# Kernel tuning notes

Hardware: AMD Instinct MI355X
Metric: run time of the kernel (lower is better)

The kernel has to match this reference:

```python
import jax, jax.numpy as jnp
import numpy as np

NUM_EMBEDDINGS = 8192
EMBEDDING_DIM = 512
BETA = 0.25


def setup_inputs() -> dict:
    key = jax.random.key(0)
    k1, k2 = jax.random.split(key)
    x = jax.random.normal(k1, (16, 1024, EMBEDDING_DIM), dtype=jnp.float32)
    # torch.nn.init.uniform_ -> U[0, 1)
    embeddings = jax.random.uniform(k2, (NUM_EMBEDDINGS, EMBEDDING_DIM), dtype=jnp.float32)
    return {"x": x, "embeddings": embeddings}


def reference(x, embeddings):
    input_shape = x.shape
    flat = x.reshape(-1, EMBEDDING_DIM)                      # [N, D]
    sim = jnp.matmul(flat, embeddings.T)                     # [N, K]
    s1 = jnp.sum(flat * flat, axis=1, keepdims=True)         # [N, 1]
    s2 = jnp.sum(embeddings * embeddings, axis=1)            # [K]
    distances = s1 + s2 - 2.0 * sim                          # [N, K]
    idx = jnp.argmin(distances, axis=1)                      # [N]
    # direct gather (math-equivalent to one-hot @ codebook)
    quantized = embeddings[idx].reshape(input_shape)
    sg = jax.lax.stop_gradient
    commitment_loss = BETA * jnp.mean((sg(quantized) - x) ** 2)
    codebook_loss = jnp.mean((quantized - sg(x)) ** 2)
    loss = commitment_loss + codebook_loss
    out = x + sg(quantized - x)                              # straight-through
    return (out, quantized, loss)
```

## Files before the change

### kernel.cpp

```cpp
#include <hip/hip_runtime.h>

#define DIM 512
#define N_ROWS 16384
#define K_CODES 8192
#define BK 32
#define TM 128
#define TN 128
#define NG (K_CODES / TN)
#define OUT_ELEMS (N_ROWS * DIM)
#define MARGIN 0.125f
#define RESCAN_CHUNK 1024
#define RESCAN_NCHUNK (K_CODES / RESCAN_CHUNK)
#define RESCAN_ROWS 8
#define NT (DIM / BK)

typedef _Float16 f16;
typedef _Float16 f16x8 __attribute__((ext_vector_type(8)));
typedef float f32x4 __attribute__((ext_vector_type(4)));

__device__ __forceinline__ unsigned long long pack_di(float d, int i) {
  unsigned u = __float_as_uint(d);
  u = (u & 0x80000000u) ? ~u : (u | 0x80000000u);
  return ((unsigned long long)u << 32) | (unsigned)i;
}

__global__ __launch_bounds__(256) void vq_split_kernel(const float* __restrict__ src,
                                                       f16* __restrict__ x16) {
  int i = (blockIdx.x * 256 + threadIdx.x) * 8;
  float4 v0 = *(const float4*)(src + i);
  float4 v1 = *(const float4*)(src + i + 4);
  float f[8] = {v0.x, v0.y, v0.z, v0.w, v1.x, v1.y, v1.z, v1.w};
  f16x8 h;
  #pragma unroll
  for (int j = 0; j < 8; ++j) h[j] = (f16)f[j];
  *(f16x8*)(x16 + i) = h;
}

__global__ __launch_bounds__(256) void vq_split_enorm_kernel(
    const float* __restrict__ emb, f16* __restrict__ e16,
    float* __restrict__ enorm, int* __restrict__ counter) {
  int gid  = blockIdx.x * 256 + threadIdx.x;
  if (gid == 0) *counter = 0;
  int code = gid >> 6;
  int lane = gid & 63;
  size_t off = (size_t)code * DIM + lane * 8;
  float4 v0 = *(const float4*)(emb + off);
  float4 v1 = *(const float4*)(emb + off + 4);
  float f[8] = {v0.x, v0.y, v0.z, v0.w, v1.x, v1.y, v1.z, v1.w};
  f16x8 h;
  float s = 0.0f;
  #pragma unroll
  for (int j = 0; j < 8; ++j) {
    h[j] = (f16)f[j];
    s = fmaf(f[j], f[j], s);
  }
  *(f16x8*)(e16 + off) = h;
  #pragma unroll
  for (int o = 32; o > 0; o >>= 1) s += __shfl_down(s, o);
  if (lane == 0) enorm[code] = s;
}

__device__ __forceinline__ void gl2lds16(const f16* g, f16* l) {
  __builtin_amdgcn_global_load_lds((const __attribute__((address_space(1))) unsigned int*)g,
                                   (__attribute__((address_space(3))) unsigned int*)l,
                                   16, 0, 0);
}

__device__ __forceinline__ void top2_merge(float& d1, int& i1, float& d2,
                                           float od1, int oi1, float od2) {
  if (od1 < d1 || (od1 == d1 && oi1 < i1)) {
    d2 = fminf(d1, od2);
    d1 = od1; i1 = oi1;
  } else {
    d2 = fminf(d2, od1);
  }
}

__global__ __launch_bounds__(256, 4) void vq_argmin_mfma_kernel(
    const f16* __restrict__ x16, const f16* __restrict__ e16,
    const float* __restrict__ enorm,
    float* __restrict__ cand_d1, int* __restrict__ cand_i1, float* __restrict__ cand_d2) {
  __shared__ __align__(16) f16 Ax[2][TM * BK];
  __shared__ __align__(16) f16 Be[2][TN * BK];
  __shared__ float red_d1[2][TM];
  __shared__ int   red_i1[2][TM];
  __shared__ float red_d2[2][TM];

  const int tid  = threadIdx.x;
  const int wave = tid >> 6;
  const int lane = tid & 63;
  const int bm = blockIdx.x, bn = blockIdx.y;
  const int wr = (wave >> 1) * 64;
  const int wc = (wave & 1) * 64;

  const f16* gsrc0;
  int ldoff;
  {
    const int srow = lane >> 2;
    const int scg  = ((lane & 3) ^ ((lane >> 3) & 3)) * 8;
    const int rowoff = (wave & 1) * 64;
    if (wave < 2) { gsrc0 = x16 + (size_t)(bm * TM + rowoff + srow) * DIM + scg; }
    else          { gsrc0 = e16 + (size_t)(bn * TN + rowoff + srow) * DIM + scg; }
    ldoff = rowoff * BK;
  }
  f16* dstA0 = (wave < 2) ? &Ax[0][ldoff] : &Be[0][ldoff];
  f16* dstA1 = (wave < 2) ? &Ax[1][ldoff] : &Be[1][ldoff];

  f32x4 acc[4][4];
  #pragma unroll
  for (int i = 0; i < 4; ++i)
    #pragma unroll
    for (int j = 0; j < 4; ++j)
      acc[i][j] = (f32x4){0.f, 0.f, 0.f, 0.f};

  const int fr = lane & 15;
  const int fq = lane >> 4;
  const int sw8 = (fq ^ ((fr >> 1) & 3)) * 8;

  #pragma unroll
  for (int i = 0; i < 4; ++i)
    gl2lds16(gsrc0 + (size_t)(16 * i) * DIM, dstA0 + (16 * i) * BK);
  __syncthreads();

  #pragma unroll 2
  for (int s = 0; s < NT; ++s) {
    const int cur = s & 1;
    if (s + 1 < NT) {
      f16* nb = cur ? dstA0 : dstA1;
      const int k1 = (s + 1) * BK;
      #pragma unroll
      for (int i = 0; i < 4; ++i)
        gl2lds16(gsrc0 + (size_t)(16 * i) * DIM + k1, nb + (16 * i) * BK);
    }

    const f16* A = cur ? &Ax[1][0] : &Ax[0][0];
    const f16* B = cur ? &Be[1][0] : &Be[0][0];
    f16x8 a[4], b[4];
    #pragma unroll
    for (int f = 0; f < 4; ++f) {
      a[f] = *(const f16x8*)&A[(wr + f * 16 + fr) * BK + sw8];
      b[f] = *(const f16x8*)&B[(wc + f * 16 + fr) * BK + sw8];
    }
    #pragma unroll
    for (int mf = 0; mf < 4; ++mf)
      #pragma unroll
      for (int nf = 0; nf < 4; ++nf)
        acc[mf][nf] = __builtin_amdgcn_mfma_f32_16x16x32_f16(a[mf], b[nf], acc[mf][nf], 0, 0, 0);

    __syncthreads();
  }

  float en[4];
  #pragma unroll
  for (int nf = 0; nf < 4; ++nf)
    en[nf] = enorm[bn * TN + wc + nf * 16 + fr];

  #pragma unroll
  for (int mf = 0; mf < 4; ++mf) {
    #pragma unroll
    for (int reg = 0; reg < 4; ++reg) {
      float d1 = 3.4e38f, d2 = 3.4e38f;
      int i1 = 0;
      #pragma unroll
      for (int nf = 0; nf < 4; ++nf) {
        float d = en[nf] - 2.0f * acc[mf][nf][reg];
        int ci = bn * TN + wc + nf * 16 + fr;
        if (d < d1) { d2 = d1; d1 = d; i1 = ci; }
        else if (d < d2) { d2 = d; }
      }
      #pragma unroll
      for (int m = 1; m <= 8; m <<= 1) {
        float od1 = __shfl_xor(d1, m, 16);
        int   oi1 = __shfl_xor(i1, m, 16);
        float od2 = __shfl_xor(d2, m, 16);
        top2_merge(d1, i1, d2, od1, oi1, od2);
      }
      if (fr == 0) {
        int row = wr + mf * 16 + fq * 4 + reg;
        red_d1[wave & 1][row] = d1;
        red_i1[wave & 1][row] = i1;
        red_d2[wave & 1][row] = d2;
      }
    }
  }
  __syncthreads();
  if (tid < TM) {
    float d1 = red_d1[0][tid]; int i1 = red_i1[0][tid]; float d2 = red_d2[0][tid];
    top2_merge(d1, i1, d2, red_d1[1][tid], red_i1[1][tid], red_d2[1][tid]);
    size_t o = (size_t)bn * N_ROWS + (size_t)bm * TM + tid;
    cand_d1[o] = d1; cand_i1[o] = i1; cand_d2[o] = d2;
  }
}

__global__ __launch_bounds__(256) void vq_merge2_kernel(
    const float* __restrict__ cd1, const int* __restrict__ ci1, const float* __restrict__ cd2,
    int* __restrict__ idx, int* __restrict__ flag,
    int* __restrict__ counter, int* __restrict__ flagged,
    unsigned long long* __restrict__ packed,
    float* __restrict__ loss_slot) {
  int r = blockIdx.x * 256 + threadIdx.x;
  if (r == 0) *loss_slot = 0.0f;
  float d1 = 3.4e38f, d2 = 3.4e38f;
  int i1 = 0;
  for (int g = 0; g < NG; ++g) {
    size_t o = (size_t)g * N_ROWS + r;
    top2_merge(d1, i1, d2, cd1[o], ci1[o], cd2[o]);
  }
  idx[r] = i1;
  int f = (d2 - d1 < MARGIN) ? 1 : 0;
  flag[r] = f;
  if (f) {
    packed[r] = 0xFFFFFFFFFFFFFFFFULL;
    int slot = atomicAdd(counter, 1);
    flagged[slot] = r;
  }
}

__global__ __launch_bounds__(256) void vq_rescan_kernel(
    const float* __restrict__ x, const float* __restrict__ emb,
    const float* __restrict__ enorm,
    const int* __restrict__ counter, const int* __restrict__ flagged,
    unsigned long long* __restrict__ packed) {
  __shared__ float4 xs[RESCAN_ROWS][DIM / 4];
  __shared__ unsigned long long wmin[4][RESCAN_ROWS];
  const int t  = threadIdx.x;
  const int wv = t >> 6, ln = t & 63;
  const int nflag   = counter[0];
  const int ngroups = (nflag + RESCAN_ROWS - 1) / RESCAN_ROWS;
  const int nitems  = ngroups * RESCAN_NCHUNK;
  for (int item = blockIdx.x; item < nitems; item += gridDim.x) {
    const int g  = item / RESCAN_NCHUNK;
    const int c0 = (item % RESCAN_NCHUNK) * RESCAN_CHUNK;
    __syncthreads();
    #pragma unroll
    for (int u = 0; u < 4; ++u) {
      int i4 = u * 256 + t;
      int j = i4 >> 7, k = i4 & 127;
      int rj = g * RESCAN_ROWS + j;
      if (rj < nflag) xs[j][k] = ((const float4*)(x + (size_t)flagged[rj] * DIM))[k];
    }
    __syncthreads();
    unsigned long long best[RESCAN_ROWS];
    #pragma unroll
    for (int j = 0; j < RESCAN_ROWS; ++j) best[j] = ~0ULL;
    #pragma unroll
    for (int cc = 0; cc < RESCAN_CHUNK / 256; ++cc) {
      const int c = c0 + cc * 256 + t;
      const float4* e4 = (const float4*)(emb + (size_t)c * DIM);
      float s0[RESCAN_ROWS], s1[RESCAN_ROWS], s2[RESCAN_ROWS], s3[RESCAN_ROWS];
      #pragma unroll
      for (int j = 0; j < RESCAN_ROWS; ++j) { s0[j] = s1[j] = s2[j] = s3[j] = 0.f; }
      for (int k = 0; k < DIM / 4; ++k) {
        float4 ev = e4[k];
        #pragma unroll
        for (int j = 0; j < RESCAN_ROWS; ++j) {
          float4 xv = xs[j][k];
          s0[j] = fmaf(xv.x, ev.x, s0[j]);
          s1[j] = fmaf(xv.y, ev.y, s1[j]);
          s2[j] = fmaf(xv.z, ev.z, s2[j]);
          s3[j] = fmaf(xv.w, ev.w, s3[j]);
        }
      }
      const float en = enorm[c];
      #pragma unroll
      for (int j = 0; j < RESCAN_ROWS; ++j) {
        float d = en - 2.0f * ((s0[j] + s1[j]) + (s2[j] + s3[j]));
        unsigned long long p = pack_di(d, c);
        if (p < best[j]) best[j] = p;
      }
    }
    #pragma unroll
    for (int j = 0; j < RESCAN_ROWS; ++j) {
      #pragma unroll
      for (int off = 32; off > 0; off >>= 1) {
        unsigned long long o = __shfl_down(best[j], off);
        if (o < best[j]) best[j] = o;
      }
    }
    if (ln == 0) {
      #pragma unroll
      for (int j = 0; j < RESCAN_ROWS; ++j) wmin[wv][j] = best[j];
    }
    __syncthreads();
    if (t < RESCAN_ROWS) {
      int rj = g * RESCAN_ROWS + t;
      if (rj < nflag) {
        unsigned long long m = wmin[0][t];
        if (wmin[1][t] < m) m = wmin[1][t];
        if (wmin[2][t] < m) m = wmin[2][t];
        if (wmin[3][t] < m) m = wmin[3][t];
        atomicMin(&packed[flagged[rj]], m);
      }
    }
  }
}

__global__ __launch_bounds__(256) void vq_gather_kernel(
    const float* __restrict__ x, const float* __restrict__ emb,
    const int* __restrict__ idx, const int* __restrict__ flag,
    const unsigned long long* __restrict__ packed,
    float* __restrict__ out, float* __restrict__ quant,
    float* __restrict__ loss_slot) {
  __shared__ float wsum[4];
  const int wave = threadIdx.x >> 6;
  const int lane = threadIdx.x & 63;
  const int row  = blockIdx.x * 4 + wave;
  const int code = flag[row] ? (int)(packed[row] & 0xFFFFFFFFu) : idx[row];
  const float4* xp = (const float4*)(x   + (size_t)row  * DIM + lane * 8);
  const float4* ep = (const float4*)(emb + (size_t)code * DIM + lane * 8);
  float s = 0.0f;
  #pragma unroll
  for (int t = 0; t < 2; ++t) {
    float4 xv = xp[t];
    float4 ev = ep[t];
    float dx = ev.x - xv.x, dy = ev.y - xv.y, dz = ev.z - xv.z, dw = ev.w - xv.w;
    s += dx * dx + dy * dy + dz * dz + dw * dw;
    ((float4*)(out   + (size_t)row * DIM + lane * 8))[t] = ev;
    ((float4*)(quant + (size_t)row * DIM + lane * 8))[t] = ev;
  }
  #pragma unroll
  for (int off = 32; off > 0; off >>= 1) s += __shfl_down(s, off);
  if (lane == 0) wsum[wave] = s;
  __syncthreads();
  if (threadIdx.x == 0) {
    float tot = wsum[0] + wsum[1] + wsum[2] + wsum[3];
    atomicAdd(loss_slot, tot * (1.25f / (float)OUT_ELEMS));
  }
}

extern "C" void kernel_launch(void* const* d_in, const int* in_sizes, int n_in,
                              void* d_out, int out_size, void* d_ws, size_t ws_size,
                              hipStream_t stream) {
  const float* x   = (const float*)d_in[0];
  const float* emb = (const float*)d_in[1];
  float* out   = (float*)d_out;
  float* quant = out + OUT_ELEMS;
  float* loss  = out + 2 * OUT_ELEMS;

  char* ws = (char*)d_ws;
  f16*   x16    = (f16*)(ws);
  f16*   e16    = (f16*)(ws + 16777216);
  float* enorm  = (float*)(ws + 25165824);
  float* cd1    = (float*)(ws + 25198592);
  int*   ci1    = (int*)  (ws + 29392896);
  float* cd2    = (float*)(ws + 33587200);
  int*   idx    = (int*)  (ws + 37781504);
  int*   flag   = (int*)  (ws + 37847040);
  int*   counter= (int*)  (ws + 37912576);
  int*   flagged= (int*)  (ws + 37912832);
  unsigned long long* packed = (unsigned long long*)(ws + 37978368);

  vq_split_kernel<<<OUT_ELEMS / (8 * 256), 256, 0, stream>>>(x, x16);
  vq_split_enorm_kernel<<<K_CODES * 64 / 256, 256, 0, stream>>>(emb, e16, enorm, counter);
  vq_argmin_mfma_kernel<<<dim3(N_ROWS / TM, K_CODES / TN), 256, 0, stream>>>(
      x16, e16, enorm, cd1, ci1, cd2);
  vq_merge2_kernel<<<N_ROWS / 256, 256, 0, stream>>>(
      cd1, ci1, cd2, idx, flag, counter, flagged, packed, loss);
  vq_rescan_kernel<<<2048, 256, 0, stream>>>(x, emb, enorm, counter, flagged, packed);
  vq_gather_kernel<<<N_ROWS / 4, 256, 0, stream>>>(x, emb, idx, flag, packed, out, quant, loss);
}
```

Before: 533.8 us.

## Load X fragments directly from global into registers, stage only codebook in LDS

The A operand (input rows) is no longer staged through shared memory. Each wave now loads its own MFMA fragments straight from global memory into registers, double-buffered with a prefetch of the next K slice. The codebook tile still goes through LDS, with all four waves sharing the async copy. This cuts LDS footprint and LDS read traffic, which could improve occupancy, but adds uncoalesced-ish 16-byte global loads per lane that are duplicated across the two waves sharing the same rows, plus extra register pressure.

```diff
diff --git a/kernel.cpp b/kernel.cpp
--- a/kernel.cpp
+++ b/kernel.cpp
@@ -80,7 +80,6 @@
     const f16* __restrict__ x16, const f16* __restrict__ e16,
     const float* __restrict__ enorm,
     float* __restrict__ cand_d1, int* __restrict__ cand_i1, float* __restrict__ cand_d2) {
-  __shared__ __align__(16) f16 Ax[2][TM * BK];
   __shared__ __align__(16) f16 Be[2][TN * BK];
   __shared__ float red_d1[2][TM];
   __shared__ int   red_i1[2][TM];
@@ -93,60 +92,63 @@
   const int wr = (wave >> 1) * 64;
   const int wc = (wave & 1) * 64;
 
-  const f16* gsrc0;
-  int ldoff;
+  const f16* gB;
   {
     const int srow = lane >> 2;
     const int scg  = ((lane & 3) ^ ((lane >> 3) & 3)) * 8;
-    const int rowoff = (wave & 1) * 64;
-    if (wave < 2) { gsrc0 = x16 + (size_t)(bm * TM + rowoff + srow) * DIM + scg; }
-    else          { gsrc0 = e16 + (size_t)(bn * TN + rowoff + srow) * DIM + scg; }
-    ldoff = rowoff * BK;
-  }
-  f16* dstA0 = (wave < 2) ? &Ax[0][ldoff] : &Be[0][ldoff];
-  f16* dstA1 = (wave < 2) ? &Ax[1][ldoff] : &Be[1][ldoff];
-
-  f32x4 acc[4][4];
-  #pragma unroll
-  for (int i = 0; i < 4; ++i)
-    #pragma unroll
-    for (int j = 0; j < 4; ++j)
-      acc[i][j] = (f32x4){0.f, 0.f, 0.f, 0.f};
+    gB = e16 + (size_t)(bn * TN + wave * 32 + srow) * DIM + scg;
+  }
+  f16* dstB0 = &Be[0][wave * 32 * BK];
+  f16* dstB1 = &Be[1][wave * 32 * BK];
 
   const int fr = lane & 15;
   const int fq = lane >> 4;
   const int sw8 = (fq ^ ((fr >> 1) & 3)) * 8;
 
+  unsigned aidx[4];
+  #pragma unroll
+  for (int f = 0; f < 4; ++f)
+    aidx[f] = (unsigned)(bm * TM + wr + f * 16 + fr) * DIM + fq * 8;
+
+  f32x4 acc[4][4];
   #pragma unroll
   for (int i = 0; i < 4; ++i)
-    gl2lds16(gsrc0 + (size_t)(16 * i) * DIM, dstA0 + (16 * i) * BK);
+    #pragma unroll
+    for (int j = 0; j < 4; ++j)
+      acc[i][j] = (f32x4){0.f, 0.f, 0.f, 0.f};
+
+  gl2lds16(gB,            dstB0);
+  gl2lds16(gB + 16 * DIM, dstB0 + 16 * BK);
+  f16x8 aC[4], aN[4];
+  #pragma unroll
+  for (int f = 0; f < 4; ++f) aC[f] = *(const f16x8*)(x16 + aidx[f]);
   __syncthreads();
 
   #pragma unroll 2
   for (int s = 0; s < NT; ++s) {
     const int cur = s & 1;
     if (s + 1 < NT) {
-      f16* nb = cur ? dstA0 : dstA1;
-      const int k1 = (s + 1) * BK;
-      #pragma unroll
-      for (int i = 0; i < 4; ++i)
-        gl2lds16(gsrc0 + (size_t)(16 * i) * DIM + k1, nb + (16 * i) * BK);
-    }
-
-    const f16* A = cur ? &Ax[1][0] : &Ax[0][0];
+      f16* nb = cur ? dstB0 : dstB1;
+      gl2lds16(gB + (s + 1) * BK,            nb);
+      gl2lds16(gB + (s + 1) * BK + 16 * DIM, nb + 16 * BK);
+      #pragma unroll
+      for (int f = 0; f < 4; ++f)
+        aN[f] = *(const f16x8*)(x16 + aidx[f] + (s + 1) * BK);
+    }
+
     const f16* B = cur ? &Be[1][0] : &Be[0][0];
-    f16x8 a[4], b[4];
-    #pragma unroll
-    for (int f = 0; f < 4; ++f) {
-      a[f] = *(const f16x8*)&A[(wr + f * 16 + fr) * BK + sw8];
+    f16x8 b[4];
+    #pragma unroll
+    for (int f = 0; f < 4; ++f)
       b[f] = *(const f16x8*)&B[(wc + f * 16 + fr) * BK + sw8];
-    }
     #pragma unroll
     for (int mf = 0; mf < 4; ++mf)
       #pragma unroll
       for (int nf = 0; nf < 4; ++nf)
-        acc[mf][nf] = __builtin_amdgcn_mfma_f32_16x16x32_f16(a[mf], b[nf], acc[mf][nf], 0, 0, 0);
-
+        acc[mf][nf] = __builtin_amdgcn_mfma_f32_16x16x32_f16(aC[mf], b[nf], acc[mf][nf], 0, 0, 0);
+
+    #pragma unroll
+    for (int f = 0; f < 4; ++f) aC[f] = aN[f];
     __syncthreads();
   }
 
```

Measured after the change: 615.3 us. 15.3% more time.

## Add split-fp16 MFMA refinement stage to shrink fp32 rescan set

Applied to the files above, without the earlier changes.

Rows whose top-2 margin is ambiguous are now compacted and re-scored with a three-term hi/lo fp16 MFMA product (near-fp32 accuracy) instead of going straight to the slow scalar fp32 rescan. Only rows still within a much tighter margin go to the fp32 rescan, which is meant to cut the expensive per-row full-codebook scalar pass. It adds a compact kernel, a refine GEMM over up to CAP rows, and a second merge. It also writes a low-part codebook. Rows beyond CAP fall back to the fp16 argmin, which risks wrong indices if many rows are flagged.

```diff
diff --git a/kernel.cpp b/kernel.cpp
--- a/kernel.cpp
+++ b/kernel.cpp
@@ -9,6 +9,8 @@
 #define NG (K_CODES / TN)
 #define OUT_ELEMS (N_ROWS * DIM)
 #define MARGIN 0.125f
+#define MARGIN2 0.004f
+#define CAP 4096
 #define RESCAN_CHUNK 1024
 #define RESCAN_NCHUNK (K_CODES / RESCAN_CHUNK)
 #define RESCAN_ROWS 8
@@ -37,24 +39,27 @@
 }
 
 __global__ __launch_bounds__(256) void vq_split_enorm_kernel(
-    const float* __restrict__ emb, f16* __restrict__ e16,
-    float* __restrict__ enorm, int* __restrict__ counter) {
+    const float* __restrict__ emb, f16* __restrict__ eh, f16* __restrict__ el,
+    float* __restrict__ enorm, int* __restrict__ counter, int* __restrict__ rcounter) {
   int gid  = blockIdx.x * 256 + threadIdx.x;
-  if (gid == 0) *counter = 0;
+  if (gid == 0) { *counter = 0; *rcounter = 0; }
   int code = gid >> 6;
   int lane = gid & 63;
   size_t off = (size_t)code * DIM + lane * 8;
   float4 v0 = *(const float4*)(emb + off);
   float4 v1 = *(const float4*)(emb + off + 4);
   float f[8] = {v0.x, v0.y, v0.z, v0.w, v1.x, v1.y, v1.z, v1.w};
-  f16x8 h;
+  f16x8 h, l;
   float s = 0.0f;
   #pragma unroll
   for (int j = 0; j < 8; ++j) {
-    h[j] = (f16)f[j];
+    f16 hj = (f16)f[j];
+    h[j] = hj;
+    l[j] = (f16)(f[j] - (float)hj);
     s = fmaf(f[j], f[j], s);
   }
-  *(f16x8*)(e16 + off) = h;
+  *(f16x8*)(eh + off) = h;
+  *(f16x8*)(el + off) = l;
   #pragma unroll
   for (int o = 32; o > 0; o >>= 1) s += __shfl_down(s, o);
   if (lane == 0) enorm[code] = s;
@@ -196,7 +201,6 @@
     const float* __restrict__ cd1, const int* __restrict__ ci1, const float* __restrict__ cd2,
     int* __restrict__ idx, int* __restrict__ flag,
     int* __restrict__ counter, int* __restrict__ flagged,
-    unsigned long long* __restrict__ packed,
     float* __restrict__ loss_slot) {
   int r = blockIdx.x * 256 + threadIdx.x;
   if (r == 0) *loss_slot = 0.0f;
@@ -207,26 +211,192 @@
     top2_merge(d1, i1, d2, cd1[o], ci1[o], cd2[o]);
   }
   idx[r] = i1;
-  int f = (d2 - d1 < MARGIN) ? 1 : 0;
-  flag[r] = f;
-  if (f) {
-    packed[r] = 0xFFFFFFFFFFFFFFFFULL;
+  if (d2 - d1 < MARGIN) {
     int slot = atomicAdd(counter, 1);
+    flag[r] = slot + 1;
     flagged[slot] = r;
+  } else {
+    flag[r] = 0;
+  }
+}
+
+__global__ __launch_bounds__(256) void vq_compact_kernel(
+    const float* __restrict__ x, const int* __restrict__ counter,
+    const int* __restrict__ flagged,
+    f16* __restrict__ xch, f16* __restrict__ xcl) {
+  const int slot = blockIdx.x * 4 + (threadIdx.x >> 6);
+  const int lane = threadIdx.x & 63;
+  int nf = counter[0]; if (nf > CAP) nf = CAP;
+  size_t doff = (size_t)slot * DIM + lane * 8;
+  f16x8 h, l;
+  if (slot < nf) {
+    const int r = flagged[slot];
+    size_t soff = (size_t)r * DIM + lane * 8;
+    float4 v0 = *(const float4*)(x + soff);
+    float4 v1 = *(const float4*)(x + soff + 4);
+    float f[8] = {v0.x, v0.y, v0.z, v0.w, v1.x, v1.y, v1.z, v1.w};
+    #pragma unroll
+    for (int j = 0; j < 8; ++j) {
+      f16 hj = (f16)f[j];
+      h[j] = hj;
+      l[j] = (f16)(f[j] - (float)hj);
+    }
+  } else {
+    #pragma unroll
+    for (int j = 0; j < 8; ++j) { h[j] = (f16)0.f; l[j] = (f16)0.f; }
+  }
+  *(f16x8*)(xch + doff) = h;
+  *(f16x8*)(xcl + doff) = l;
+}
+
+__global__ __launch_bounds__(256, 4) void vq_refine_kernel(
+    const f16* __restrict__ xch, const f16* __restrict__ xcl,
+    const f16* __restrict__ eh, const f16* __restrict__ el,
+    const float* __restrict__ enorm, const int* __restrict__ counter,
+    float* __restrict__ cd1b, int* __restrict__ ci1b, float* __restrict__ cd2b) {
+  __shared__ __align__(16) f16 Axh[TM * BK];
+  __shared__ __align__(16) f16 Axl[TM * BK];
+  __shared__ __align__(16) f16 Beh[TN * BK];
+  __shared__ __align__(16) f16 Bel[TN * BK];
+  __shared__ float red_d1[2][TM];
+  __shared__ int   red_i1[2][TM];
+  __shared__ float red_d2[2][TM];
+
+  const int tid  = threadIdx.x;
+  const int wave = tid >> 6;
+  const int lane = tid & 63;
+  const int bm = blockIdx.x, bn = blockIdx.y;
+  int nflag = counter[0]; if (nflag > CAP) nflag = CAP;
+  if (bm * TM >= nflag) return;
+
+  const int wr = (wave >> 1) * 64;
+  const int wc = (wave & 1) * 64;
+
+  const f16* gsrc0;
+  f16* ldst;
+  {
+    const int srow = lane >> 2;
+    const int scol = ((lane & 3) ^ ((lane >> 3) & 3)) * 8;
+    if (wave == 0)      { gsrc0 = xch + (size_t)(bm * TM + srow) * DIM + scol; ldst = Axh; }
+    else if (wave == 1) { gsrc0 = xcl + (size_t)(bm * TM + srow) * DIM + scol; ldst = Axl; }
+    else if (wave == 2) { gsrc0 = eh  + (size_t)(bn * TN + srow) * DIM + scol; ldst = Beh; }
+    else                { gsrc0 = el  + (size_t)(bn * TN + srow) * DIM + scol; ldst = Bel; }
+  }
+
+  f32x4 acc[4][4];
+  #pragma unroll
+  for (int i = 0; i < 4; ++i)
+    #pragma unroll
+    for (int j = 0; j < 4; ++j)
+      acc[i][j] = (f32x4){0.f, 0.f, 0.f, 0.f};
+
+  const int fr = lane & 15;
+  const int fq = lane >> 4;
+  const int sw8 = (fq ^ ((fr >> 1) & 3)) * 8;
+
+  for (int k0 = 0; k0 < DIM; k0 += BK) {
+    __syncthreads();
+    #pragma unroll
+    for (int i = 0; i < 8; ++i)
+      gl2lds16(gsrc0 + (size_t)(16 * i) * DIM + k0, ldst + (16 * i) * BK);
+    __syncthreads();
+
+    f16x8 ah[4], al[4], bh[4], bl[4];
+    #pragma unroll
+    for (int f = 0; f < 4; ++f) {
+      ah[f] = *(const f16x8*)&Axh[(wr + f * 16 + fr) * BK + sw8];
+      al[f] = *(const f16x8*)&Axl[(wr + f * 16 + fr) * BK + sw8];
+      bh[f] = *(const f16x8*)&Beh[(wc + f * 16 + fr) * BK + sw8];
+      bl[f] = *(const f16x8*)&Bel[(wc + f * 16 + fr) * BK + sw8];
+    }
+    #pragma unroll
+    for (int mf = 0; mf < 4; ++mf)
+      #pragma unroll
+      for (int nf = 0; nf < 4; ++nf) {
+        acc[mf][nf] = __builtin_amdgcn_mfma_f32_16x16x32_f16(ah[mf], bh[nf], acc[mf][nf], 0, 0, 0);
+        acc[mf][nf] = __builtin_amdgcn_mfma_f32_16x16x32_f16(ah[mf], bl[nf], acc[mf][nf], 0, 0, 0);
+        acc[mf][nf] = __builtin_amdgcn_mfma_f32_16x16x32_f16(al[mf], bh[nf], acc[mf][nf], 0, 0, 0);
+      }
+  }
+
+  float en[4];
+  #pragma unroll
+  for (int nf = 0; nf < 4; ++nf)
+    en[nf] = enorm[bn * TN + wc + nf * 16 + fr];
+
+  #pragma unroll
+  for (int mf = 0; mf < 4; ++mf) {
+    #pragma unroll
+    for (int reg = 0; reg < 4; ++reg) {
+      float d1 = 3.4e38f, d2 = 3.4e38f;
+      int i1 = 0;
+      #pragma unroll
+      for (int nf = 0; nf < 4; ++nf) {
+        float d = en[nf] - 2.0f * acc[mf][nf][reg];
+        int ci = bn * TN + wc + nf * 16 + fr;
+        if (d < d1) { d2 = d1; d1 = d; i1 = ci; }
+        else if (d < d2) { d2 = d; }
+      }
+      #pragma unroll
+      for (int m = 1; m <= 8; m <<= 1) {
+        float od1 = __shfl_xor(d1, m, 16);
+        int   oi1 = __shfl_xor(i1, m, 16);
+        float od2 = __shfl_xor(d2, m, 16);
+        top2_merge(d1, i1, d2, od1, oi1, od2);
+      }
+      if (fr == 0) {
+        int row = wr + mf * 16 + fq * 4 + reg;
+        red_d1[wave & 1][row] = d1;
+        red_i1[wave & 1][row] = i1;
+        red_d2[wave & 1][row] = d2;
+      }
+    }
+  }
+  __syncthreads();
+  if (tid < TM) {
+    float d1 = red_d1[0][tid]; int i1 = red_i1[0][tid]; float d2 = red_d2[0][tid];
+    top2_merge(d1, i1, d2, red_d1[1][tid], red_i1[1][tid], red_d2[1][tid]);
+    size_t o = (size_t)bn * CAP + (size_t)bm * TM + tid;
+    cd1b[o] = d1; ci1b[o] = i1; cd2b[o] = d2;
+  }
+}
+
+__global__ __launch_bounds__(256) void vq_merge2b_kernel(
+    const float* __restrict__ cd1b, const int* __restrict__ ci1b, const float* __restrict__ cd2b,
+    const int* __restrict__ counter,
+    int* __restrict__ idxR, int* __restrict__ flagR,
+    int* __restrict__ rcounter, int* __restrict__ rlist,
+    unsigned long long* __restrict__ packed) {
+  int s = blockIdx.x * 256 + threadIdx.x;
+  float d1 = 3.4e38f, d2 = 3.4e38f;
+  int i1 = 0;
+  for (int g = 0; g < NG; ++g) {
+    size_t o = (size_t)g * CAP + s;
+    top2_merge(d1, i1, d2, cd1b[o], ci1b[o], cd2b[o]);
+  }
+  idxR[s] = i1;
+  int f2 = (d2 - d1 < MARGIN2) ? 1 : 0;
+  flagR[s] = f2;
+  int nf = counter[0]; if (nf > CAP) nf = CAP;
+  if (s < nf && f2) {
+    int rs = atomicAdd(rcounter, 1);
+    rlist[rs] = s;
+    packed[s] = 0xFFFFFFFFFFFFFFFFULL;
   }
 }
 
 __global__ __launch_bounds__(256) void vq_rescan_kernel(
     const float* __restrict__ x, const float* __restrict__ emb,
     const float* __restrict__ enorm,
-    const int* __restrict__ counter, const int* __restrict__ flagged,
+    const int* __restrict__ rcounter, const int* __restrict__ rlist,
+    const int* __restrict__ flagged,
     unsigned long long* __restrict__ packed) {
   __shared__ float4 xs[RESCAN_ROWS][DIM / 4];
   __shared__ unsigned long long wmin[4][RESCAN_ROWS];
   const int t  = threadIdx.x;
   const int wv = t >> 6, ln = t & 63;
-  const int nflag   = counter[0];
-  const int ngroups = (nflag + RESCAN_ROWS - 1) / RESCAN_ROWS;
+  const int rcnt    = rcounter[0];
+  const int ngroups = (rcnt + RESCAN_ROWS - 1) / RESCAN_ROWS;
   const int nitems  = ngroups * RESCAN_NCHUNK;
   for (int item = blockIdx.x; item < nitems; item += gridDim.x) {
     const int g  = item / RESCAN_NCHUNK;
@@ -235,9 +405,9 @@
     #pragma unroll
     for (int u = 0; u < 4; ++u) {
       int i4 = u * 256 + t;
-      int j = i4 >> 7, k = i4 & 127;
+      int j = i4 >> 7, kk = i4 & 127;
       int rj = g * RESCAN_ROWS + j;
-      if (rj < nflag) xs[j][k] = ((const float4*)(x + (size_t)flagged[rj] * DIM))[k];
+      if (rj < rcnt) xs[j][kk] = ((const float4*)(x + (size_t)flagged[rlist[rj]] * DIM))[kk];
     }
     __syncthreads();
     unsigned long long best[RESCAN_ROWS];
@@ -284,12 +454,12 @@
     __syncthreads();
     if (t < RESCAN_ROWS) {
       int rj = g * RESCAN_ROWS + t;
-      if (rj < nflag) {
+      if (rj < rcnt) {
         unsigned long long m = wmin[0][t];
         if (wmin[1][t] < m) m = wmin[1][t];
         if (wmin[2][t] < m) m = wmin[2][t];
         if (wmin[3][t] < m) m = wmin[3][t];
-        atomicMin(&packed[flagged[rj]], m);
+        atomicMin(&packed[rlist[rj]], m);
       }
     }
   }
@@ -298,6 +468,7 @@
 __global__ __launch_bounds__(256) void vq_gather_kernel(
     const float* __restrict__ x, const float* __restrict__ emb,
     const int* __restrict__ idx, const int* __restrict__ flag,
+    const int* __restrict__ flagR, const int* __restrict__ idxR,
     const unsigned long long* __restrict__ packed,
     float* __restrict__ out, float* __restrict__ quant,
     float* __restrict__ loss_slot) {
@@ -305,7 +476,15 @@
   const int wave = threadIdx.x >> 6;
   const int lane = threadIdx.x & 63;
   const int row  = blockIdx.x * 4 + wave;
-  const int code = flag[row] ? (int)(packed[row] & 0xFFFFFFFFu) : idx[row];
+  const int f    = flag[row];
+  int code;
+  if (f == 0) {
+    code = idx[row];
+  } else {
+    int slot = f - 1;
+    if (slot >= CAP) code = idx[row];
+    else code = flagR[slot] ? (int)(packed[slot] & 0xFFFFFFFFu) : idxR[slot];
+  }
   const float4* xp = (const float4*)(x   + (size_t)row  * DIM + lane * 8);
   const float4* ep = (const float4*)(emb + (size_t)code * DIM + lane * 8);
   float s = 0.0f;
@@ -340,22 +519,38 @@
   char* ws = (char*)d_ws;
   f16*   x16    = (f16*)(ws);
   f16*   e16    = (f16*)(ws + 16777216);
-  float* enorm  = (float*)(ws + 25165824);
-  float* cd1    = (float*)(ws + 25198592);
-  int*   ci1    = (int*)  (ws + 29392896);
-  float* cd2    = (float*)(ws + 33587200);
-  int*   idx    = (int*)  (ws + 37781504);
-  int*   flag   = (int*)  (ws + 37847040);
-  int*   counter= (int*)  (ws + 37912576);
-  int*   flagged= (int*)  (ws + 37912832);
-  unsigned long long* packed = (unsigned long long*)(ws + 37978368);
+  f16*   ecl    = (f16*)(ws + 25165824);
+  float* enorm  = (float*)(ws + 33554432);
+  float* cd1    = (float*)(ws + 33619968);
+  int*   ci1    = (int*)  (ws + 37814272);
+  float* cd2    = (float*)(ws + 42008576);
+  int*   idx    = (int*)  (ws + 46202880);
+  int*   flag   = (int*)  (ws + 46268416);
+  int*   flagged= (int*)  (ws + 46333952);
+  int*   counter= (int*)  (ws + 46399488);
+  int*   rcounter=(int*)  (ws + 46399616);
+  f16*   xch    = (f16*)(ws + 46399744);
+  f16*   xcl    = (f16*)(ws + 50594048);
+  float* cd1b   = (float*)(ws + 54788352);
+  int*   ci1b   = (int*)  (ws + 55836928);
+  float* cd2b   = (float*)(ws + 56885504);
+  int*   idxR   = (int*)  (ws + 57934080);
+  int*   flagR  = (int*)  (ws + 57950464);
+  int*   rlist  = (int*)  (ws + 57966848);
+  unsigned long long* packed = (unsigned long long*)(ws + 57983232);
 
   vq_split_kernel<<<OUT_ELEMS / (8 * 256), 256, 0, stream>>>(x, x16);
-  vq_split_enorm_kernel<<<K_CODES * 64 / 256, 256, 0, stream>>>(emb, e16, enorm, counter);
+  vq_split_enorm_kernel<<<K_CODES * 64 / 256, 256, 0, stream>>>(emb, e16, ecl, enorm, counter, rcounter);
   vq_argmin_mfma_kernel<<<dim3(N_ROWS / TM, K_CODES / TN), 256, 0, stream>>>(
       x16, e16, enorm, cd1, ci1, cd2);
   vq_merge2_kernel<<<N_ROWS / 256, 256, 0, stream>>>(
-      cd1, ci1, cd2, idx, flag, counter, flagged, packed, loss);
-  vq_rescan_kernel<<<2048, 256, 0, stream>>>(x, emb, enorm, counter, flagged, packed);
-  vq_gather_kernel<<<N_ROWS / 4, 256, 0, stream>>>(x, emb, idx, flag, packed, out, quant, loss);
-}
+      cd1, ci1, cd2, idx, flag, counter, flagged, loss);
+  vq_compact_kernel<<<CAP / 4, 256, 0, stream>>>(x, counter, flagged, xch, xcl);
+  vq_refine_kernel<<<dim3(CAP / TM, K_CODES / TN), 256, 0, stream>>>(
+      xch, xcl, e16, ecl, enorm, counter, cd1b, ci1b, cd2b);
+  vq_merge2b_kernel<<<CAP / 256, 256, 0, stream>>>(
+      cd1b, ci1b, cd2b, counter, idxR, flagR, rcounter, rlist, packed);
+  vq_rescan_kernel<<<2048, 256, 0, stream>>>(x, emb, enorm, rcounter, rlist, flagged, packed);
+  vq_gather_kernel<<<N_ROWS / 4, 256, 0, stream>>>(
+      x, emb, idx, flag, flagR, idxR, packed, out, quant, loss);
+}
```

New measurement: 645.3 us. 1.21x slower.
